# Performance work log

Measured on AMD Instinct MI355X. Metric: run time of the kernel, lower is better.

The kernel has to match this reference:

```python
import jax, jax.numpy as jnp
import numpy as np

TAU = 1.5
SCALE = 0.125
EPS = 1e-5
H = 8

@jax.custom_vjp
def spike(u):
    return (u >= 0.0).astype(u.dtype)

def _spike_fwd(u):
    return spike(u), u

def _spike_bwd(u, g):
    # ATan surrogate gradient, alpha=2 (spikingjelly default)
    return (g / (1.0 + (jnp.pi * u) ** 2),)

spike.defvjp(_spike_fwd, _spike_bwd)

def lif_ms(xt):
    # xt: (T, ...) multi-step LIF, decay_input=True, v_th=1, hard reset to 0, detach_reset
    def step(v, x):
        v = v + (x - v) / TAU
        s = spike(v - 1.0)
        v = v * (1.0 - jax.lax.stop_gradient(s))
        return v, s
    _, s = jax.lax.scan(step, jnp.zeros_like(xt[0]), xt)
    return s

def bn(x, g, b, m, var):
    # eval-mode BatchNorm1d over channel dim of (B, C, L)
    inv = g / jnp.sqrt(var + EPS)
    return (x - m[None, :, None]) * inv[None, :, None] + b[None, :, None]

def setup_inputs() -> dict:
    key = jax.random.key(0)
    ks = jax.random.split(key, 16)
    B, C, T, N = 8, 512, 4, 256
    w_scale = 1.0 / np.sqrt(C)
    inp = {
        'x': jax.random.normal(ks[0], (B, C, T, N), jnp.float32),
        'wq': jax.random.normal(ks[1], (C, C), jnp.float32) * w_scale,
        'wk': jax.random.normal(ks[2], (C, C), jnp.float32) * w_scale,
        'wv': jax.random.normal(ks[3], (C, C), jnp.float32) * w_scale,
        'wp': jax.random.normal(ks[4], (C, C), jnp.float32) * w_scale,
        'bp': jnp.zeros((C,), jnp.float32),
        'gq': jax.random.uniform(ks[5], (C,), jnp.float32, 0.5, 1.5),
        'bq': jax.random.uniform(ks[6], (C,), jnp.float32),
        'mq': jnp.zeros((C,), jnp.float32),
        'vq': jnp.ones((C,), jnp.float32),
        'gk': jax.random.uniform(ks[7], (C,), jnp.float32, 0.5, 1.5),
        'bk': jax.random.uniform(ks[8], (C,), jnp.float32),
        'mk': jnp.zeros((C,), jnp.float32),
        'vk': jnp.ones((C,), jnp.float32),
        'gv': jax.random.uniform(ks[9], (C,), jnp.float32, 0.5, 1.5),
        'bv': jax.random.uniform(ks[10], (C,), jnp.float32),
        'mv': jnp.zeros((C,), jnp.float32),
        'vv': jnp.ones((C,), jnp.float32),
        'gp': jax.random.uniform(ks[11], (C,), jnp.float32, 0.5, 1.5),
        'bpn': jax.random.uniform(ks[12], (C,), jnp.float32),
        'mp': jnp.zeros((C,), jnp.float32),
        'vp': jnp.ones((C,), jnp.float32),
    }
    return inp

def reference(x, wq, wk, wv, wp, bp, gq, bq, mq, vq, gk, bk, mk, vk,
              gv, bv, mv, vv, gp, bpn, mp, vp):
    B, C, T, N = x.shape
    L = T * N
    d = C // H

    # proj_bn then multi-step proj_lif over time dim
    xb = bn(x.reshape(B, C, L), gp, bpn, mp, vp).reshape(B, C, T, N)
    s0 = lif_ms(jnp.transpose(xb, (2, 0, 1, 3)))            # (T,B,C,N)
    x_for_qkv = jnp.transpose(s0, (1, 2, 0, 3)).reshape(B, C, L)  # (B,C,L)

    def qkv_branch(w, g, b_, m, v_):
        y = bn(jnp.einsum('oc,bcl->bol', w, x_for_qkv), g, b_, m, v_)
        y = y.reshape(B, C, T, N)
        sy = lif_ms(jnp.transpose(y, (2, 0, 1, 3)))         # (T,B,C,N)
        sy = jnp.transpose(sy, (1, 0, 3, 2)).reshape(B, L, C)  # (B,T,N,C)->(B,L,C)
        return jnp.transpose(sy.reshape(B, L, H, d), (0, 2, 1, 3))  # (B,H,L,d)

    q = qkv_branch(wq, gq, bq, mq, vq)
    k = qkv_branch(wk, gk, bk, mk, vk)
    v = qkv_branch(wv, gv, bv, mv, vv)

    attn = jnp.einsum('bhqd,bhkd->bhqk', q, k)              # no softmax
    o = jnp.einsum('bhqk,bhkd->bhqd', attn, v) * SCALE
    o = jnp.transpose(o, (0, 1, 3, 2)).reshape(B, C, L)

    # single-step attn_lif: v = o/tau from zero state, spike at threshold 1
    s = spike(o / TAU - 1.0)

    out = jnp.einsum('oc,bcl->bol', wp, s) + bp[None, :, None]
    return out.reshape(B, C, T, N)
```

## Files before the change

### kernel.cpp

```cpp
#include <hip/hip_runtime.h>
#include <hip/hip_bf16.h>


#define NB 8
#define NC 512
#define NT 4
#define NN 256
#define NL 1024
#define NH 8
#define ND 64
#define BCL (NB*NC*NL)

typedef __attribute__((ext_vector_type(8))) short  short8v;
typedef __attribute__((ext_vector_type(8))) unsigned short us8;
typedef __attribute__((ext_vector_type(4))) unsigned short us4;
typedef __attribute__((ext_vector_type(4))) float f32x4;

__device__ __forceinline__ float bu2f(unsigned short u) {
  return __uint_as_float(((unsigned)u) << 16);
}
__device__ __forceinline__ unsigned short f2bu(float f) {
  unsigned b = __float_as_uint(f);
  return (unsigned short)((b + 0x7FFFu + ((b >> 16) & 1u)) >> 16);
}

__global__ void k_prep(const float* __restrict__ wq, const float* __restrict__ wk,
                       const float* __restrict__ wv, const float* __restrict__ wp,
                       const float* __restrict__ x,
                       const float* __restrict__ g,  const float* __restrict__ bt,
                       const float* __restrict__ mu, const float* __restrict__ var,
                       unsigned short* __restrict__ H2,
                       unsigned short* __restrict__ ST0) {
  if (blockIdx.x < 512) {
    int gi = blockIdx.x * 256 + threadIdx.x;
    int p = gi >> 15;
    int o = (gi >> 6) & 511;
    int k8 = gi & 63;
    int rt = o >> 7, r = o & 127;
    int k0i = k8 >> 3, chunk = k8 & 7;
    const float* W = (p == 0) ? wq : (p == 1) ? wk : (p == 2) ? wv : wp;
    const float* src = W + (size_t)o * NC + k8 * 8;
    us8 a[3];
#pragma unroll
    for (int i = 0; i < 8; i++) {
      float w = src[i];
      unsigned short u1 = f2bu(w);
      float r1 = w - bu2f(u1);
      unsigned short u2 = f2bu(r1);
      float r2 = r1 - bu2f(u2);
      unsigned short u3 = f2bu(r2);
      a[0][i] = u1; a[1][i] = u2; a[2][i] = u3;
    }
#pragma unroll
    for (int j = 0; j < 3; j++) {
      size_t off = ((size_t)((((p * 3 + j) * 4 + rt) * 8 + k0i) * 8 + chunk)) * 1024
                   + (size_t)r * 8;
      *(us8*)&H2[off] = a[j];
    }
  } else {
    int bidx = blockIdx.x - 512;
    int b  = bidx >> 6;
    int c0 = (bidx & 63) * 8;
    int n  = threadIdx.x;
    unsigned short spk[NT][8];
#pragma unroll
    for (int i = 0; i < 8; i++) {
      int c = c0 + i;
      float inv = g[c] / sqrtf(var[c] + 1e-5f);
      float m = mu[c], be = bt[c];
      const float* xp = x + ((size_t)(b * NC + c)) * NL + n;
      float v = 0.f;
#pragma unroll
      for (int t = 0; t < NT; t++) {
        float y = (xp[t * NN] - m) * inv + be;
        v = v + (y - v) / 1.5f;
        unsigned short s = 0;
        if (v - 1.0f >= 0.f) { s = 0x3F80; v = 0.f; }
        spk[t][i] = s;
      }
    }
#pragma unroll
    for (int t = 0; t < NT; t++) {
      us8 pk;
#pragma unroll
      for (int i = 0; i < 8; i++) pk[i] = spk[t][i];
      *(us8*)&ST0[((size_t)b * NL + t * NN + n) * NC + c0] = pk;
    }
  }
}

__global__ __launch_bounds__(256) void
k_qkv(const unsigned short* __restrict__ H2,
      const unsigned short* __restrict__ ST0,
      const float* __restrict__ gq, const float* __restrict__ bq,
      const float* __restrict__ mq, const float* __restrict__ vq,
      const float* __restrict__ gk, const float* __restrict__ bk,
      const float* __restrict__ mk, const float* __restrict__ vk,
      const float* __restrict__ gv, const float* __restrict__ bv,
      const float* __restrict__ mv, const float* __restrict__ vv,
      unsigned short* __restrict__ STq, unsigned short* __restrict__ STk,
      unsigned short* __restrict__ STv) {
  __shared__ __align__(16) unsigned short sB[2][128 * 64];

  int id = blockIdx.x;
  int n0 = (id & 7) * 32;
  int rt = (id >> 3) & 3;
  int b  = (id >> 5) & 7;
  int p  = id >> 8;

  int tid = threadIdx.x;
  int w = tid >> 6, lane = tid & 63, quad = lane >> 4, l15 = lane & 15;
  int xorv = l15 & 7;

  const unsigned short* Sb = ST0 + (size_t)b * NL * NC;
  const unsigned short* Hbase = H2 + ((size_t)((p * 3) * 4 + rt) * 8) * 8192;

  f32x4 acc[2][8];
#pragma unroll
  for (int ri = 0; ri < 2; ri++)
#pragma unroll
    for (int jj = 0; jj < 8; jj++) acc[ri][jj] = (f32x4){0.f, 0.f, 0.f, 0.f};

  us8 breg[4];
  int ccs[4], segs[4];
  size_t bsrc[4];
#pragma unroll
  for (int i = 0; i < 4; i++) {
    int idx = tid + i * 256;
    int cc = idx >> 3, seg = idx & 7;
    int t = (cc >> 4) & 3, nn = (cc & 15) | ((cc >> 6) << 4);
    ccs[i] = cc; segs[i] = seg;
    bsrc[i] = (size_t)(t * NN + n0 + nn) * NC + seg * 8;
  }
#pragma unroll
  for (int i = 0; i < 4; i++) breg[i] = *(const us8*)&Sb[bsrc[i]];
#pragma unroll
  for (int i = 0; i < 4; i++)
    *(us8*)&sB[0][ccs[i] * 64 + ((segs[i] ^ (ccs[i] & 7)) << 3)] = breg[i];

  for (int k0i = 0; k0i < 8; k0i++) {
    __syncthreads();
    int buf = k0i & 1;

    short8v Ar[2][3][2];
#pragma unroll
    for (int ks = 0; ks < 2; ks++) {
      int c8 = ks * 4 + quad;
#pragma unroll
      for (int j = 0; j < 3; j++) {
        const unsigned short* Hj =
            Hbase + ((size_t)j * 4 * 8 + k0i) * 8192 + (size_t)c8 * 1024;
        Ar[ks][j][0] = *(const short8v*)&Hj[(w * 32 + l15) * 8];
        Ar[ks][j][1] = *(const short8v*)&Hj[(w * 32 + 16 + l15) * 8];
      }
    }
    if (k0i < 7) {
#pragma unroll
      for (int i = 0; i < 4; i++)
        breg[i] = *(const us8*)&Sb[bsrc[i] + (size_t)(k0i + 1) * 64];
    }
#pragma unroll
    for (int ks = 0; ks < 2; ks++) {
      int c8 = ks * 4 + quad;
      int poff = (c8 ^ xorv) << 3;
      short8v bf[8];
#pragma unroll
      for (int jj = 0; jj < 8; jj++)
        bf[jj] = *(const short8v*)&sB[buf][(jj * 16 + l15) * 64 + poff];
#pragma unroll
      for (int j = 0; j < 3; j++) {
#pragma unroll
        for (int jj = 0; jj < 8; jj++) {
          acc[0][jj] = __builtin_amdgcn_mfma_f32_16x16x32_bf16(Ar[ks][j][0], bf[jj], acc[0][jj], 0, 0, 0);
          acc[1][jj] = __builtin_amdgcn_mfma_f32_16x16x32_bf16(Ar[ks][j][1], bf[jj], acc[1][jj], 0, 0, 0);
        }
      }
    }
    if (k0i < 7) {
#pragma unroll
      for (int i = 0; i < 4; i++)
        *(us8*)&sB[buf ^ 1][ccs[i] * 64 + ((segs[i] ^ (ccs[i] & 7)) << 3)] = breg[i];
    }
  }

  const float *g, *bb, *mm, *vr;
  unsigned short* So;
  if (p == 0)      { g = gq; bb = bq; mm = mq; vr = vq; So = STq; }
  else if (p == 1) { g = gk; bb = bk; mm = mk; vr = vk; So = STk; }
  else             { g = gv; bb = bv; mm = mv; vr = vv; So = STv; }
  So += (size_t)b * NL * NC;

#pragma unroll
  for (int ri = 0; ri < 2; ri++) {
    int ob = rt * 128 + w * 32 + ri * 16 + quad * 4;
    float av[4], mvv[4], bvv[4];
#pragma unroll
    for (int r = 0; r < 4; r++) {
      av[r]  = g[ob + r] / sqrtf(vr[ob + r] + 1e-5f);
      mvv[r] = mm[ob + r];
      bvv[r] = bb[ob + r];
    }
#pragma unroll
    for (int nh = 0; nh < 2; nh++) {
      int n = n0 + (nh << 4) + l15;
      unsigned short sp[4][4];
#pragma unroll
      for (int r = 0; r < 4; r++) {
        float vmem = 0.f;
#pragma unroll
        for (int t = 0; t < NT; t++) {
          float y = (acc[ri][nh * 4 + t][r] - mvv[r]) * av[r] + bvv[r];
          vmem = vmem + (y - vmem) / 1.5f;
          unsigned short s = 0;
          if (vmem - 1.0f >= 0.f) { s = 0x3F80; vmem = 0.f; }
          sp[t][r] = s;
        }
      }
#pragma unroll
      for (int t = 0; t < NT; t++) {
        us4 pk;
#pragma unroll
        for (int r = 0; r < 4; r++) pk[r] = sp[t][r];
        *(us4*)&So[(size_t)(t * NN + n) * NC + ob] = pk;
      }
    }
  }
}

__global__ void k_kvM(const unsigned short* __restrict__ STk,
                      const unsigned short* __restrict__ STv,
                      float* __restrict__ Mpart) {
  int bh = blockIdx.x, ch = blockIdx.y;
  int b = bh >> 3, h = bh & 7;
  const unsigned short* Kp = STk + (size_t)b * NL * NC + h * ND;
  const unsigned short* Vp = STv + (size_t)b * NL * NC + h * ND;
  __shared__ float sK[64][72];
  __shared__ float sV[64][72];
  int tid = threadIdx.x, tx = tid & 15, ty = tid >> 4;
  float acc[4][4] = {};
  for (int lt = 0; lt < 2; lt++) {
    int lb = ch * 128 + lt * 64;
#pragma unroll
    for (int i = 0; i < 2; i++) {
      int idx = tid + i * 256;
      int r = idx >> 3, seg = idx & 7;
      us8 kv = *(const us8*)&Kp[(size_t)(lb + r) * NC + seg * 8];
      us8 vv = *(const us8*)&Vp[(size_t)(lb + r) * NC + seg * 8];
#pragma unroll
      for (int q2 = 0; q2 < 8; q2++) {
        sK[r][seg * 8 + q2] = bu2f(kv[q2]);
        sV[r][seg * 8 + q2] = bu2f(vv[q2]);
      }
    }
    __syncthreads();
#pragma unroll 8
    for (int lc = 0; lc < 64; lc++) {
      float kvx[4], vvx[4];
#pragma unroll
      for (int i = 0; i < 4; i++) kvx[i] = sK[lc][ty * 4 + i];
#pragma unroll
      for (int j2 = 0; j2 < 4; j2++) vvx[j2] = sV[lc][tx * 4 + j2];
#pragma unroll
      for (int i = 0; i < 4; i++)
#pragma unroll
        for (int j2 = 0; j2 < 4; j2++)
          acc[i][j2] += kvx[i] * vvx[j2];
    }
    __syncthreads();
  }
  float* Mp = Mpart + ((size_t)ch * 64 + bh) * 4096;
#pragma unroll
  for (int i = 0; i < 4; i++) {
    float4 v4 = make_float4(acc[i][0], acc[i][1], acc[i][2], acc[i][3]);
    *(float4*)&Mp[(ty * 4 + i) * ND + tx * 4] = v4;
  }
}

__global__ __launch_bounds__(256) void
k_attn(const unsigned short* __restrict__ STq,
       const float* __restrict__ Mpart,
       unsigned short* __restrict__ STs) {
  __shared__ unsigned short MT1[64 * 64];
  __shared__ unsigned short MT2[64 * 64];
  int lt = blockIdx.x, bh = blockIdx.y;
  int b = bh >> 3, h = bh & 7;
  int tid = threadIdx.x;
  int w = tid >> 6, lane = tid & 63, quad = lane >> 4, l15 = lane & 15;

#pragma unroll
  for (int i = 0; i < 4; i++) {
    int idx4 = tid + i * 256;
    float4 s = ((const float4*)Mpart)[(size_t)bh * 1024 + idx4];
#pragma unroll
    for (int ch = 1; ch < 8; ch++) {
      float4 t = ((const float4*)Mpart)[((size_t)ch * 64 + bh) * 1024 + idx4];
      s.x += t.x; s.y += t.y; s.z += t.z; s.w += t.w;
    }
    int e = idx4 >> 4;
    int dd0 = (idx4 * 4) & 63;
    int chunk = e >> 3;
    float sv[4] = {s.x, s.y, s.z, s.w};
#pragma unroll
    for (int r = 0; r < 4; r++) {
      int dd = dd0 + r;
      unsigned short u1 = f2bu(sv[r]);
      unsigned short u2 = f2bu(sv[r] - bu2f(u1));
      int pos = dd * 64 + (((chunk ^ (dd & 7)) << 3) | (e & 7));
      MT1[pos] = u1;
      MT2[pos] = u2;
    }
  }
  __syncthreads();

  const unsigned short* Qp = STq + (size_t)b * NL * NC + h * ND;
  int lbase = lt * 256 + w * 64;

  f32x4 acc[4][4];
#pragma unroll
  for (int dt = 0; dt < 4; dt++)
#pragma unroll
    for (int j = 0; j < 4; j++) acc[dt][j] = (f32x4){0.f, 0.f, 0.f, 0.f};

#pragma unroll
  for (int ks = 0; ks < 2; ks++) {
    short8v bq[4];
#pragma unroll
    for (int ltile = 0; ltile < 4; ltile++)
      bq[ltile] = *(const short8v*)&Qp[(size_t)(lbase + ltile * 16 + l15) * NC
                                       + ks * 32 + quad * 8];
    int c8 = ks * 4 + quad;
#pragma unroll
    for (int dt = 0; dt < 4; dt++) {
      int dd = dt * 16 + l15;
      int off = dd * 64 + ((c8 ^ (dd & 7)) << 3);
      short8v a1 = *(const short8v*)&MT1[off];
      short8v a2 = *(const short8v*)&MT2[off];
#pragma unroll
      for (int ltile = 0; ltile < 4; ltile++) {
        acc[dt][ltile] = __builtin_amdgcn_mfma_f32_16x16x32_bf16(a1, bq[ltile], acc[dt][ltile], 0, 0, 0);
        acc[dt][ltile] = __builtin_amdgcn_mfma_f32_16x16x32_bf16(a2, bq[ltile], acc[dt][ltile], 0, 0, 0);
      }
    }
  }

  unsigned short* Sp = STs + (size_t)b * NL * NC + h * ND;
#pragma unroll
  for (int dt = 0; dt < 4; dt++)
#pragma unroll
    for (int ltile = 0; ltile < 4; ltile++) {
      int l = lbase + ltile * 16 + l15;
      int dd = dt * 16 + quad * 4;
      us4 pk;
#pragma unroll
      for (int r = 0; r < 4; r++) pk[r] = (acc[dt][ltile][r] >= 12.0f) ? 0x3F80 : 0;
      *(us4*)&Sp[(size_t)l * NC + dd] = pk;
    }
}

__global__ __launch_bounds__(256) void
k_out(const unsigned short* __restrict__ H2,
      const unsigned short* __restrict__ STs,
      const float* __restrict__ bp, float* __restrict__ out) {
  __shared__ __align__(16) unsigned short sB[2][64 * 64];

  int id = blockIdx.x;
  int l0 = (id & 15) * 64;
  int rt = (id >> 4) & 3;
  int b  = id >> 6;

  int tid = threadIdx.x;
  int w = tid >> 6, lane = tid & 63, quad = lane >> 4, l15 = lane & 15;
  int xorv = l15 & 7;

  const unsigned short* Sb = STs + (size_t)b * NL * NC;
  const unsigned short* Hbase = H2 + ((size_t)(9 * 4 + rt) * 8) * 8192;

  f32x4 acc[2][4];
#pragma unroll
  for (int ri = 0; ri < 2; ri++)
#pragma unroll
    for (int jj = 0; jj < 4; jj++) acc[ri][jj] = (f32x4){0.f, 0.f, 0.f, 0.f};

  us8 breg[2];
  int ccs[2], segs[2];
  size_t bsrc[2];
#pragma unroll
  for (int i = 0; i < 2; i++) {
    int idx = tid + i * 256;
    int cc = idx >> 3, seg = idx & 7;
    ccs[i] = cc; segs[i] = seg;
    bsrc[i] = (size_t)(l0 + cc) * NC + seg * 8;
  }
#pragma unroll
  for (int i = 0; i < 2; i++) breg[i] = *(const us8*)&Sb[bsrc[i]];
#pragma unroll
  for (int i = 0; i < 2; i++)
    *(us8*)&sB[0][ccs[i] * 64 + ((segs[i] ^ (ccs[i] & 7)) << 3)] = breg[i];

  for (int k0i = 0; k0i < 8; k0i++) {
    __syncthreads();
    int buf = k0i & 1;

    short8v Ar[2][3][2];
#pragma unroll
    for (int ks = 0; ks < 2; ks++) {
      int c8 = ks * 4 + quad;
#pragma unroll
      for (int j = 0; j < 3; j++) {
        const unsigned short* Hj =
            Hbase + ((size_t)j * 4 * 8 + k0i) * 8192 + (size_t)c8 * 1024;
        Ar[ks][j][0] = *(const short8v*)&Hj[(w * 32 + l15) * 8];
        Ar[ks][j][1] = *(const short8v*)&Hj[(w * 32 + 16 + l15) * 8];
      }
    }
    if (k0i < 7) {
#pragma unroll
      for (int i = 0; i < 2; i++)
        breg[i] = *(const us8*)&Sb[bsrc[i] + (size_t)(k0i + 1) * 64];
    }
#pragma unroll
    for (int ks = 0; ks < 2; ks++) {
      int c8 = ks * 4 + quad;
      int poff = (c8 ^ xorv) << 3;
      short8v bf[4];
#pragma unroll
      for (int jj = 0; jj < 4; jj++)
        bf[jj] = *(const short8v*)&sB[buf][(jj * 16 + l15) * 64 + poff];
#pragma unroll
      for (int j = 0; j < 3; j++) {
#pragma unroll
        for (int jj = 0; jj < 4; jj++) {
          acc[0][jj] = __builtin_amdgcn_mfma_f32_16x16x32_bf16(Ar[ks][j][0], bf[jj], acc[0][jj], 0, 0, 0);
          acc[1][jj] = __builtin_amdgcn_mfma_f32_16x16x32_bf16(Ar[ks][j][1], bf[jj], acc[1][jj], 0, 0, 0);
        }
      }
    }
    if (k0i < 7) {
#pragma unroll
      for (int i = 0; i < 2; i++)
        *(us8*)&sB[buf ^ 1][ccs[i] * 64 + ((segs[i] ^ (ccs[i] & 7)) << 3)] = breg[i];
    }
  }

#pragma unroll
  for (int ri = 0; ri < 2; ri++) {
    int ob = rt * 128 + w * 32 + ri * 16 + quad * 4;
#pragma unroll
    for (int jj = 0; jj < 4; jj++) {
      int l = l0 + jj * 16 + l15;
#pragma unroll
      for (int r = 0; r < 4; r++)
        out[((size_t)(b * NC + ob + r)) * NL + l] = acc[ri][jj][r] + bp[ob + r];
    }
  }
}

extern "C" void kernel_launch(void* const* d_in, const int* in_sizes, int n_in,
                              void* d_out, int out_size, void* d_ws, size_t ws_size,
                              hipStream_t stream) {
  (void)in_sizes; (void)n_in; (void)out_size; (void)ws_size;
  const float* x   = (const float*)d_in[0];
  const float* wq  = (const float*)d_in[1];
  const float* wk  = (const float*)d_in[2];
  const float* wv  = (const float*)d_in[3];
  const float* wp  = (const float*)d_in[4];
  const float* bp  = (const float*)d_in[5];
  const float* gq  = (const float*)d_in[6];
  const float* bq  = (const float*)d_in[7];
  const float* mq  = (const float*)d_in[8];
  const float* vq  = (const float*)d_in[9];
  const float* gk  = (const float*)d_in[10];
  const float* bk  = (const float*)d_in[11];
  const float* mk  = (const float*)d_in[12];
  const float* vk  = (const float*)d_in[13];
  const float* gv  = (const float*)d_in[14];
  const float* bv  = (const float*)d_in[15];
  const float* mv  = (const float*)d_in[16];
  const float* vvv = (const float*)d_in[17];
  const float* gp  = (const float*)d_in[18];
  const float* bpn = (const float*)d_in[19];
  const float* mp  = (const float*)d_in[20];
  const float* vp  = (const float*)d_in[21];

  unsigned short* H2  = (unsigned short*)d_ws;
  unsigned short* ST0 = H2 + (size_t)4 * 3 * NC * NC;
  unsigned short* STq = ST0 + BCL;
  unsigned short* STk = STq + BCL;
  unsigned short* STv = STk + BCL;
  unsigned short* STs = STv + BCL;
  float* Mpart = (float*)(STs + BCL);

  dim3 blk(256);
  k_prep<<<1024, blk, 0, stream>>>(wq, wk, wv, wp, x, gp, bpn, mp, vp, H2, ST0);
  k_qkv<<<768, blk, 0, stream>>>(H2, ST0,
      gq, bq, mq, vq, gk, bk, mk, vk, gv, bv, mv, vvv, STq, STk, STv);
  k_kvM<<<dim3(64, 8), blk, 0, stream>>>(STk, STv, Mpart);
  k_attn<<<dim3(4, 64), blk, 0, stream>>>(STq, Mpart, STs);
  k_out<<<512, blk, 0, stream>>>(H2, STs, bp, (float*)d_out);
}
```

Measured before the change: 191.6 us.

## Double-buffer weight fragments in registers and remap blocks per XCD in qkv/out GEMMs

The qkv and out projection GEMMs now load the weight A fragments for the next k-step into a second register set while the current step's MFMAs run, with the k-loop fully unrolled via macros. Block indices are also remapped so consecutive block ids landing on the same XCD share a weight row-tile and batch, to improve L2 reuse. The aim is to hide global-load latency of the weight fragments and cut L2 misses. The cost is higher VGPR pressure from holding two A sets, which could lower occupancy.

```diff
diff --git a/kernel.cpp b/kernel.cpp
--- a/kernel.cpp
+++ b/kernel.cpp
@@ -103,10 +103,12 @@
   __shared__ __align__(16) unsigned short sB[2][128 * 64];
 
   int id = blockIdx.x;
-  int n0 = (id & 7) * 32;
-  int rt = (id >> 3) & 3;
-  int b  = (id >> 5) & 7;
-  int p  = id >> 8;
+  int xcd = id & 7, slot = id >> 3;
+  int qq = xcd * 96 + slot;
+  int grp = qq >> 6, mi = qq & 63;
+  int p = grp >> 2, rt = grp & 3;
+  int b = mi >> 3;
+  int n0 = (mi & 7) * 32;
 
   int tid = threadIdx.x;
   int w = tid >> 6, lane = tid & 63, quad = lane >> 4, l15 = lane & 15;
@@ -120,6 +122,21 @@
   for (int ri = 0; ri < 2; ri++)
 #pragma unroll
     for (int jj = 0; jj < 8; jj++) acc[ri][jj] = (f32x4){0.f, 0.f, 0.f, 0.f};
+
+  short8v A0[2][3][2], A1[2][3][2];
+
+#define QLOADA(DST, K0I)                                                     \
+  _Pragma("unroll") for (int ks = 0; ks < 2; ks++) {                         \
+    int c8 = ks * 4 + quad;                                                  \
+    _Pragma("unroll") for (int j = 0; j < 3; j++) {                          \
+      const unsigned short* Hj =                                             \
+          Hbase + ((size_t)(j * 4 * 8 + (K0I))) * 8192 + (size_t)c8 * 1024;  \
+      DST[ks][j][0] = *(const short8v*)&Hj[(w * 32 + l15) * 8];              \
+      DST[ks][j][1] = *(const short8v*)&Hj[(w * 32 + 16 + l15) * 8];         \
+    }                                                                        \
+  }
+
+  QLOADA(A0, 0);
 
   us8 breg[4];
   int ccs[4], segs[4];
@@ -138,56 +155,57 @@
   for (int i = 0; i < 4; i++)
     *(us8*)&sB[0][ccs[i] * 64 + ((segs[i] ^ (ccs[i] & 7)) << 3)] = breg[i];
 
-  for (int k0i = 0; k0i < 8; k0i++) {
-    __syncthreads();
-    int buf = k0i & 1;
-
-    short8v Ar[2][3][2];
-#pragma unroll
-    for (int ks = 0; ks < 2; ks++) {
-      int c8 = ks * 4 + quad;
-#pragma unroll
-      for (int j = 0; j < 3; j++) {
-        const unsigned short* Hj =
-            Hbase + ((size_t)j * 4 * 8 + k0i) * 8192 + (size_t)c8 * 1024;
-        Ar[ks][j][0] = *(const short8v*)&Hj[(w * 32 + l15) * 8];
-        Ar[ks][j][1] = *(const short8v*)&Hj[(w * 32 + 16 + l15) * 8];
-      }
-    }
-    if (k0i < 7) {
-#pragma unroll
-      for (int i = 0; i < 4; i++)
-        breg[i] = *(const us8*)&Sb[bsrc[i] + (size_t)(k0i + 1) * 64];
-    }
-#pragma unroll
-    for (int ks = 0; ks < 2; ks++) {
-      int c8 = ks * 4 + quad;
-      int poff = (c8 ^ xorv) << 3;
-      short8v bf[8];
-#pragma unroll
-      for (int jj = 0; jj < 8; jj++)
-        bf[jj] = *(const short8v*)&sB[buf][(jj * 16 + l15) * 64 + poff];
-#pragma unroll
-      for (int j = 0; j < 3; j++) {
-#pragma unroll
-        for (int jj = 0; jj < 8; jj++) {
-          acc[0][jj] = __builtin_amdgcn_mfma_f32_16x16x32_bf16(Ar[ks][j][0], bf[jj], acc[0][jj], 0, 0, 0);
-          acc[1][jj] = __builtin_amdgcn_mfma_f32_16x16x32_bf16(Ar[ks][j][1], bf[jj], acc[1][jj], 0, 0, 0);
-        }
-      }
-    }
-    if (k0i < 7) {
-#pragma unroll
-      for (int i = 0; i < 4; i++)
-        *(us8*)&sB[buf ^ 1][ccs[i] * 64 + ((segs[i] ^ (ccs[i] & 7)) << 3)] = breg[i];
-    }
-  }
-
-  const float *g, *bb, *mm, *vr;
+#define QBPRE(K0N)                                                           \
+  _Pragma("unroll") for (int i = 0; i < 4; i++)                              \
+    breg[i] = *(const us8*)&Sb[bsrc[i] + (size_t)(K0N) * 64];
+
+#define QBWRITE(BUFN)                                                        \
+  _Pragma("unroll") for (int i = 0; i < 4; i++)                              \
+    *(us8*)&sB[BUFN][ccs[i] * 64 + ((segs[i] ^ (ccs[i] & 7)) << 3)] = breg[i];
+
+#define QMFMAS(AR, BUF)                                                      \
+  _Pragma("unroll") for (int ks = 0; ks < 2; ks++) {                         \
+    int c8 = ks * 4 + quad;                                                  \
+    int poff = (c8 ^ xorv) << 3;                                             \
+    short8v bf[8];                                                           \
+    _Pragma("unroll") for (int jj = 0; jj < 8; jj++)                         \
+      bf[jj] = *(const short8v*)&sB[BUF][(jj * 16 + l15) * 64 + poff];       \
+    _Pragma("unroll") for (int j = 0; j < 3; j++)                            \
+      _Pragma("unroll") for (int jj = 0; jj < 8; jj++) {                     \
+        acc[0][jj] = __builtin_amdgcn_mfma_f32_16x16x32_bf16(                \
+            AR[ks][j][0], bf[jj], acc[0][jj], 0, 0, 0);                      \
+        acc[1][jj] = __builtin_amdgcn_mfma_f32_16x16x32_bf16(                \
+            AR[ks][j][1], bf[jj], acc[1][jj], 0, 0, 0);                      \
+      }                                                                      \
+  }
+
+#define QSTEP(K0I, ACUR, ANXT)                                               \
+  __syncthreads();                                                           \
+  { if ((K0I) < 7) { QLOADA(ANXT, (K0I) + 1); } }                            \
+  { if ((K0I) < 7) { QBPRE((K0I) + 1); } }                                   \
+  QMFMAS(ACUR, (K0I) & 1);                                                   \
+  { if ((K0I) < 7) { QBWRITE(((K0I) & 1) ^ 1); } }
+
+  QSTEP(0, A0, A1)
+  QSTEP(1, A1, A0)
+  QSTEP(2, A0, A1)
+  QSTEP(3, A1, A0)
+  QSTEP(4, A0, A1)
+  QSTEP(5, A1, A0)
+  QSTEP(6, A0, A1)
+  QSTEP(7, A1, A0)
+
+#undef QLOADA
+#undef QBPRE
+#undef QBWRITE
+#undef QMFMAS
+#undef QSTEP
+
+  const float *g, *bb, *mpt, *vr;
   unsigned short* So;
-  if (p == 0)      { g = gq; bb = bq; mm = mq; vr = vq; So = STq; }
-  else if (p == 1) { g = gk; bb = bk; mm = mk; vr = vk; So = STk; }
-  else             { g = gv; bb = bv; mm = mv; vr = vv; So = STv; }
+  if (p == 0)      { g = gq; bb = bq; mpt = mq; vr = vq; So = STq; }
+  else if (p == 1) { g = gk; bb = bk; mpt = mk; vr = vk; So = STk; }
+  else             { g = gv; bb = bv; mpt = mv; vr = vv; So = STv; }
   So += (size_t)b * NL * NC;
 
 #pragma unroll
@@ -197,7 +215,7 @@
 #pragma unroll
     for (int r = 0; r < 4; r++) {
       av[r]  = g[ob + r] / sqrtf(vr[ob + r] + 1e-5f);
-      mvv[r] = mm[ob + r];
+      mvv[r] = mpt[ob + r];
       bvv[r] = bb[ob + r];
     }
 #pragma unroll
@@ -364,9 +382,12 @@
   __shared__ __align__(16) unsigned short sB[2][64 * 64];
 
   int id = blockIdx.x;
-  int l0 = (id & 15) * 64;
-  int rt = (id >> 4) & 3;
-  int b  = id >> 6;
+  int xcd = id & 7, slot = id >> 3;
+  int qq = xcd * 64 + slot;
+  int rt = qq >> 7;
+  int mi = qq & 127;
+  int b  = mi >> 4;
+  int l0 = (mi & 15) * 64;
 
   int tid = threadIdx.x;
   int w = tid >> 6, lane = tid & 63, quad = lane >> 4, l15 = lane & 15;
@@ -380,6 +401,21 @@
   for (int ri = 0; ri < 2; ri++)
 #pragma unroll
     for (int jj = 0; jj < 4; jj++) acc[ri][jj] = (f32x4){0.f, 0.f, 0.f, 0.f};
+
+  short8v A0[2][3][2], A1[2][3][2];
+
+#define OLOADA(DST, K0I)                                                     \
+  _Pragma("unroll") for (int ks = 0; ks < 2; ks++) {                         \
+    int c8 = ks * 4 + quad;                                                  \
+    _Pragma("unroll") for (int j = 0; j < 3; j++) {                          \
+      const unsigned short* Hj =                                             \
+          Hbase + ((size_t)(j * 4 * 8 + (K0I))) * 8192 + (size_t)c8 * 1024;  \
+      DST[ks][j][0] = *(const short8v*)&Hj[(w * 32 + l15) * 8];              \
+      DST[ks][j][1] = *(const short8v*)&Hj[(w * 32 + 16 + l15) * 8];         \
+    }                                                                        \
+  }
+
+  OLOADA(A0, 0);
 
   us8 breg[2];
   int ccs[2], segs[2];
@@ -397,50 +433,51 @@
   for (int i = 0; i < 2; i++)
     *(us8*)&sB[0][ccs[i] * 64 + ((segs[i] ^ (ccs[i] & 7)) << 3)] = breg[i];
 
-  for (int k0i = 0; k0i < 8; k0i++) {
-    __syncthreads();
-    int buf = k0i & 1;
-
-    short8v Ar[2][3][2];
-#pragma unroll
-    for (int ks = 0; ks < 2; ks++) {
-      int c8 = ks * 4 + quad;
-#pragma unroll
-      for (int j = 0; j < 3; j++) {
-        const unsigned short* Hj =
-            Hbase + ((size_t)j * 4 * 8 + k0i) * 8192 + (size_t)c8 * 1024;
-        Ar[ks][j][0] = *(const short8v*)&Hj[(w * 32 + l15) * 8];
-        Ar[ks][j][1] = *(const short8v*)&Hj[(w * 32 + 16 + l15) * 8];
-      }
-    }
-    if (k0i < 7) {
-#pragma unroll
-      for (int i = 0; i < 2; i++)
-        breg[i] = *(const us8*)&Sb[bsrc[i] + (size_t)(k0i + 1) * 64];
-    }
-#pragma unroll
-    for (int ks = 0; ks < 2; ks++) {
-      int c8 = ks * 4 + quad;
-      int poff = (c8 ^ xorv) << 3;
-      short8v bf[4];
-#pragma unroll
-      for (int jj = 0; jj < 4; jj++)
-        bf[jj] = *(const short8v*)&sB[buf][(jj * 16 + l15) * 64 + poff];
-#pragma unroll
-      for (int j = 0; j < 3; j++) {
-#pragma unroll
-        for (int jj = 0; jj < 4; jj++) {
-          acc[0][jj] = __builtin_amdgcn_mfma_f32_16x16x32_bf16(Ar[ks][j][0], bf[jj], acc[0][jj], 0, 0, 0);
-          acc[1][jj] = __builtin_amdgcn_mfma_f32_16x16x32_bf16(Ar[ks][j][1], bf[jj], acc[1][jj], 0, 0, 0);
-        }
-      }
-    }
-    if (k0i < 7) {
-#pragma unroll
-      for (int i = 0; i < 2; i++)
-        *(us8*)&sB[buf ^ 1][ccs[i] * 64 + ((segs[i] ^ (ccs[i] & 7)) << 3)] = breg[i];
-    }
-  }
+#define OBPRE(K0N)                                                           \
+  _Pragma("unroll") for (int i = 0; i < 2; i++)                              \
+    breg[i] = *(const us8*)&Sb[bsrc[i] + (size_t)(K0N) * 64];
+
+#define OBWRITE(BUFN)                                                        \
+  _Pragma("unroll") for (int i = 0; i < 2; i++)                              \
+    *(us8*)&sB[BUFN][ccs[i] * 64 + ((segs[i] ^ (ccs[i] & 7)) << 3)] = breg[i];
+
+#define OMFMAS(AR, BUF)                                                      \
+  _Pragma("unroll") for (int ks = 0; ks < 2; ks++) {                         \
+    int c8 = ks * 4 + quad;                                                  \
+    int poff = (c8 ^ xorv) << 3;                                             \
+    short8v bf[4];                                                           \
+    _Pragma("unroll") for (int jj = 0; jj < 4; jj++)                         \
+      bf[jj] = *(const short8v*)&sB[BUF][(jj * 16 + l15) * 64 + poff];       \
+    _Pragma("unroll") for (int j = 0; j < 3; j++)                            \
+      _Pragma("unroll") for (int jj = 0; jj < 4; jj++) {                     \
+        acc[0][jj] = __builtin_amdgcn_mfma_f32_16x16x32_bf16(                \
+            AR[ks][j][0], bf[jj], acc[0][jj], 0, 0, 0);                      \
+        acc[1][jj] = __builtin_amdgcn_mfma_f32_16x16x32_bf16(                \
+            AR[ks][j][1], bf[jj], acc[1][jj], 0, 0, 0);                      \
+      }                                                                      \
+  }
+
+#define OSTEP(K0I, ACUR, ANXT)                                               \
+  __syncthreads();                                                           \
+  { if ((K0I) < 7) { OLOADA(ANXT, (K0I) + 1); } }                            \
+  { if ((K0I) < 7) { OBPRE((K0I) + 1); } }                                   \
+  OMFMAS(ACUR, (K0I) & 1);                                                   \
+  { if ((K0I) < 7) { OBWRITE(((K0I) & 1) ^ 1); } }
+
+  OSTEP(0, A0, A1)
+  OSTEP(1, A1, A0)
+  OSTEP(2, A0, A1)
+  OSTEP(3, A1, A0)
+  OSTEP(4, A0, A1)
+  OSTEP(5, A1, A0)
+  OSTEP(6, A0, A1)
+  OSTEP(7, A1, A0)
+
+#undef OLOADA
+#undef OBPRE
+#undef OBWRITE
+#undef OMFMAS
+#undef OSTEP
 
 #pragma unroll
   for (int ri = 0; ri < 2; ri++) {
```

After: 185.3 us. -3.3%, faster.

## Drop LDS staging in qkv/out GEMMs, load B directly, remap blocks per XCD

Applied to the files above, without the earlier changes.

The qkv and output projection kernels no longer stage the spike matrix through double-buffered shared memory with barriers. Each wave now loads its B fragments straight from global memory into registers, with the k loop fully unrolled and MFMA sections wrapped in s_setprio. Block IDs are also remapped so consecutive blocks on the same XCD share weight and batch tiles for L2 locality. This removes LDS traffic and syncs, but each of the four waves now re-reads the same B tile from global or cache, so redundant global loads go up.

```diff
diff --git a/kernel.cpp b/kernel.cpp
--- a/kernel.cpp
+++ b/kernel.cpp
@@ -100,94 +100,67 @@
       const float* __restrict__ mv, const float* __restrict__ vv,
       unsigned short* __restrict__ STq, unsigned short* __restrict__ STk,
       unsigned short* __restrict__ STv) {
-  __shared__ __align__(16) unsigned short sB[2][128 * 64];
-
   int id = blockIdx.x;
-  int n0 = (id & 7) * 32;
-  int rt = (id >> 3) & 3;
-  int b  = (id >> 5) & 7;
-  int p  = id >> 8;
+  int xcd = id & 7, slot = id >> 3;
+  int qq = xcd * 96 + slot;
+  int grp = qq >> 6, mi = qq & 63;
+  int p = grp >> 2, rt = grp & 3;
+  int b = mi >> 3;
+  int n0 = (mi & 7) * 32;
 
   int tid = threadIdx.x;
   int w = tid >> 6, lane = tid & 63, quad = lane >> 4, l15 = lane & 15;
-  int xorv = l15 & 7;
 
   const unsigned short* Sb = ST0 + (size_t)b * NL * NC;
   const unsigned short* Hbase = H2 + ((size_t)((p * 3) * 4 + rt) * 8) * 8192;
 
+  size_t brow[8];
+#pragma unroll
+  for (int jj = 0; jj < 8; jj++)
+    brow[jj] = (size_t)((jj & 3) * NN + n0 + ((jj >> 2) << 4) + l15) * NC
+               + (size_t)(quad * 8);
+
   f32x4 acc[2][8];
 #pragma unroll
   for (int ri = 0; ri < 2; ri++)
 #pragma unroll
     for (int jj = 0; jj < 8; jj++) acc[ri][jj] = (f32x4){0.f, 0.f, 0.f, 0.f};
 
-  us8 breg[4];
-  int ccs[4], segs[4];
-  size_t bsrc[4];
-#pragma unroll
-  for (int i = 0; i < 4; i++) {
-    int idx = tid + i * 256;
-    int cc = idx >> 3, seg = idx & 7;
-    int t = (cc >> 4) & 3, nn = (cc & 15) | ((cc >> 6) << 4);
-    ccs[i] = cc; segs[i] = seg;
-    bsrc[i] = (size_t)(t * NN + n0 + nn) * NC + seg * 8;
-  }
-#pragma unroll
-  for (int i = 0; i < 4; i++) breg[i] = *(const us8*)&Sb[bsrc[i]];
-#pragma unroll
-  for (int i = 0; i < 4; i++)
-    *(us8*)&sB[0][ccs[i] * 64 + ((segs[i] ^ (ccs[i] & 7)) << 3)] = breg[i];
-
-  for (int k0i = 0; k0i < 8; k0i++) {
-    __syncthreads();
-    int buf = k0i & 1;
-
-    short8v Ar[2][3][2];
+#pragma unroll
+  for (int k0 = 0; k0 < 8; k0++) {
 #pragma unroll
     for (int ks = 0; ks < 2; ks++) {
-      int c8 = ks * 4 + quad;
+      short8v bf[8];
+#pragma unroll
+      for (int jj = 0; jj < 8; jj++)
+        bf[jj] = *(const short8v*)&Sb[brow[jj] + k0 * 64 + ks * 32];
+      short8v a[3][2];
 #pragma unroll
       for (int j = 0; j < 3; j++) {
-        const unsigned short* Hj =
-            Hbase + ((size_t)j * 4 * 8 + k0i) * 8192 + (size_t)c8 * 1024;
-        Ar[ks][j][0] = *(const short8v*)&Hj[(w * 32 + l15) * 8];
-        Ar[ks][j][1] = *(const short8v*)&Hj[(w * 32 + 16 + l15) * 8];
-      }
-    }
-    if (k0i < 7) {
-#pragma unroll
-      for (int i = 0; i < 4; i++)
-        breg[i] = *(const us8*)&Sb[bsrc[i] + (size_t)(k0i + 1) * 64];
-    }
-#pragma unroll
-    for (int ks = 0; ks < 2; ks++) {
-      int c8 = ks * 4 + quad;
-      int poff = (c8 ^ xorv) << 3;
-      short8v bf[8];
-#pragma unroll
-      for (int jj = 0; jj < 8; jj++)
-        bf[jj] = *(const short8v*)&sB[buf][(jj * 16 + l15) * 64 + poff];
-#pragma unroll
-      for (int j = 0; j < 3; j++) {
+        const unsigned short* Hj = Hbase + ((size_t)(j * 32 + k0)) * 8192
+                                   + (size_t)(ks * 4 + quad) * 1024;
+        a[j][0] = *(const short8v*)&Hj[(w * 32 + l15) * 8];
+        a[j][1] = *(const short8v*)&Hj[(w * 32 + 16 + l15) * 8];
+      }
+      __builtin_amdgcn_s_setprio(1);
+#pragma unroll
+      for (int j = 0; j < 3; j++)
 #pragma unroll
         for (int jj = 0; jj < 8; jj++) {
-          acc[0][jj] = __builtin_amdgcn_mfma_f32_16x16x32_bf16(Ar[ks][j][0], bf[jj], acc[0][jj], 0, 0, 0);
-          acc[1][jj] = __builtin_amdgcn_mfma_f32_16x16x32_bf16(Ar[ks][j][1], bf[jj], acc[1][jj], 0, 0, 0);
+          acc[0][jj] = __builtin_amdgcn_mfma_f32_16x16x32_bf16(
+              a[j][0], bf[jj], acc[0][jj], 0, 0, 0);
+          acc[1][jj] = __builtin_amdgcn_mfma_f32_16x16x32_bf16(
+              a[j][1], bf[jj], acc[1][jj], 0, 0, 0);
         }
-      }
-    }
-    if (k0i < 7) {
-#pragma unroll
-      for (int i = 0; i < 4; i++)
-        *(us8*)&sB[buf ^ 1][ccs[i] * 64 + ((segs[i] ^ (ccs[i] & 7)) << 3)] = breg[i];
-    }
-  }
-
-  const float *g, *bb, *mm, *vr;
+      __builtin_amdgcn_s_setprio(0);
+    }
+  }
+
+  const float *g, *bb, *mpt, *vr;
   unsigned short* So;
-  if (p == 0)      { g = gq; bb = bq; mm = mq; vr = vq; So = STq; }
-  else if (p == 1) { g = gk; bb = bk; mm = mk; vr = vk; So = STk; }
-  else             { g = gv; bb = bv; mm = mv; vr = vv; So = STv; }
+  if (p == 0)      { g = gq; bb = bq; mpt = mq; vr = vq; So = STq; }
+  else if (p == 1) { g = gk; bb = bk; mpt = mk; vr = vk; So = STk; }
+  else             { g = gv; bb = bv; mpt = mv; vr = vv; So = STv; }
   So += (size_t)b * NL * NC;
 
 #pragma unroll
@@ -197,7 +170,7 @@
 #pragma unroll
     for (int r = 0; r < 4; r++) {
       av[r]  = g[ob + r] / sqrtf(vr[ob + r] + 1e-5f);
-      mvv[r] = mm[ob + r];
+      mvv[r] = mpt[ob + r];
       bvv[r] = bb[ob + r];
     }
 #pragma unroll
@@ -361,84 +334,58 @@
 k_out(const unsigned short* __restrict__ H2,
       const unsigned short* __restrict__ STs,
       const float* __restrict__ bp, float* __restrict__ out) {
-  __shared__ __align__(16) unsigned short sB[2][64 * 64];
-
   int id = blockIdx.x;
-  int l0 = (id & 15) * 64;
-  int rt = (id >> 4) & 3;
-  int b  = id >> 6;
+  int xcd = id & 7, slot = id >> 3;
+  int qq = xcd * 64 + slot;
+  int rt = qq >> 7;
+  int mi = qq & 127;
+  int b  = mi >> 4;
+  int l0 = (mi & 15) * 64;
 
   int tid = threadIdx.x;
   int w = tid >> 6, lane = tid & 63, quad = lane >> 4, l15 = lane & 15;
-  int xorv = l15 & 7;
 
   const unsigned short* Sb = STs + (size_t)b * NL * NC;
   const unsigned short* Hbase = H2 + ((size_t)(9 * 4 + rt) * 8) * 8192;
 
+  size_t brow[4];
+#pragma unroll
+  for (int jj = 0; jj < 4; jj++)
+    brow[jj] = (size_t)(l0 + jj * 16 + l15) * NC + (size_t)(quad * 8);
+
   f32x4 acc[2][4];
 #pragma unroll
   for (int ri = 0; ri < 2; ri++)
 #pragma unroll
     for (int jj = 0; jj < 4; jj++) acc[ri][jj] = (f32x4){0.f, 0.f, 0.f, 0.f};
 
-  us8 breg[2];
-  int ccs[2], segs[2];
-  size_t bsrc[2];
-#pragma unroll
-  for (int i = 0; i < 2; i++) {
-    int idx = tid + i * 256;
-    int cc = idx >> 3, seg = idx & 7;
-    ccs[i] = cc; segs[i] = seg;
-    bsrc[i] = (size_t)(l0 + cc) * NC + seg * 8;
-  }
-#pragma unroll
-  for (int i = 0; i < 2; i++) breg[i] = *(const us8*)&Sb[bsrc[i]];
-#pragma unroll
-  for (int i = 0; i < 2; i++)
-    *(us8*)&sB[0][ccs[i] * 64 + ((segs[i] ^ (ccs[i] & 7)) << 3)] = breg[i];
-
-  for (int k0i = 0; k0i < 8; k0i++) {
-    __syncthreads();
-    int buf = k0i & 1;
-
-    short8v Ar[2][3][2];
+#pragma unroll
+  for (int k0 = 0; k0 < 8; k0++) {
 #pragma unroll
     for (int ks = 0; ks < 2; ks++) {
-      int c8 = ks * 4 + quad;
+      short8v bf[4];
+#pragma unroll
+      for (int jj = 0; jj < 4; jj++)
+        bf[jj] = *(const short8v*)&Sb[brow[jj] + k0 * 64 + ks * 32];
+      short8v a[3][2];
 #pragma unroll
       for (int j = 0; j < 3; j++) {
-        const unsigned short* Hj =
-            Hbase + ((size_t)j * 4 * 8 + k0i) * 8192 + (size_t)c8 * 1024;
-        Ar[ks][j][0] = *(const short8v*)&Hj[(w * 32 + l15) * 8];
-        Ar[ks][j][1] = *(const short8v*)&Hj[(w * 32 + 16 + l15) * 8];
-      }
-    }
-    if (k0i < 7) {
-#pragma unroll
-      for (int i = 0; i < 2; i++)
-        breg[i] = *(const us8*)&Sb[bsrc[i] + (size_t)(k0i + 1) * 64];
-    }
-#pragma unroll
-    for (int ks = 0; ks < 2; ks++) {
-      int c8 = ks * 4 + quad;
-      int poff = (c8 ^ xorv) << 3;
-      short8v bf[4];
-#pragma unroll
-      for (int jj = 0; jj < 4; jj++)
-        bf[jj] = *(const short8v*)&sB[buf][(jj * 16 + l15) * 64 + poff];
-#pragma unroll
-      for (int j = 0; j < 3; j++) {
+        const unsigned short* Hj = Hbase + ((size_t)(j * 32 + k0)) * 8192
+                                   + (size_t)(ks * 4 + quad) * 1024;
+        a[j][0] = *(const short8v*)&Hj[(w * 32 + l15) * 8];
+        a[j][1] = *(const short8v*)&Hj[(w * 32 + 16 + l15) * 8];
+      }
+      __builtin_amdgcn_s_setprio(1);
+#pragma unroll
+      for (int j = 0; j < 3; j++)
 #pragma unroll
         for (int jj = 0; jj < 4; jj++) {
-          acc[0][jj] = __builtin_amdgcn_mfma_f32_16x16x32_bf16(Ar[ks][j][0], bf[jj], acc[0][jj], 0, 0, 0);
-          acc[1][jj] = __builtin_amdgcn_mfma_f32_16x16x32_bf16(Ar[ks][j][1], bf[jj], acc[1][jj], 0, 0, 0);
+          acc[0][jj] = __builtin_amdgcn_mfma_f32_16x16x32_bf16(
+              a[j][0], bf[jj], acc[0][jj], 0, 0, 0);
+          acc[1][jj] = __builtin_amdgcn_mfma_f32_16x16x32_bf16(
+              a[j][1], bf[jj], acc[1][jj], 0, 0, 0);
         }
-      }
-    }
-    if (k0i < 7) {
-#pragma unroll
-      for (int i = 0; i < 2; i++)
-        *(us8*)&sB[buf ^ 1][ccs[i] * 64 + ((segs[i] ^ (ccs[i] & 7)) << 3)] = breg[i];
+      __builtin_amdgcn_s_setprio(0);
     }
   }
 
```

Measured after the change: 228.5 us. 19.3% more time.
